# Kernel tuning notes

Measured on AMD Instinct MI355X. Metric: run time of the kernel, lower is better.

## Reference

```python
import jax, jax.numpy as jnp
import numpy as np

N_NODES = 100000
HIDDEN = 128
N_EDGES = 2000000
OUT_DIM = 1


def setup_inputs() -> dict:
    key = jax.random.key(0)
    k1, k2, k3, k4 = jax.random.split(key, 4)
    x_src = jax.random.normal(k1, (N_NODES, HIDDEN), dtype=jnp.float32)
    x_dst = jax.random.normal(k2, (N_NODES, HIDDEN), dtype=jnp.float32)
    edge_label_index = jax.random.randint(k3, (2, N_EDGES), 0, N_NODES, dtype=jnp.int64)
    # nn.Linear(2*hidden, out) params (Kaiming-uniform-ish init scale)
    bound = 1.0 / np.sqrt(2 * HIDDEN)
    weight = jax.random.uniform(k4, (OUT_DIM, 2 * HIDDEN), minval=-bound, maxval=bound, dtype=jnp.float32)
    bias = jnp.zeros((OUT_DIM,), dtype=jnp.float32)
    return {"x_src": x_src, "x_dst": x_dst, "edge_label_index": edge_label_index,
            "weight": weight, "bias": bias}


def reference(x_src, x_dst, edge_label_index, weight, bias):
    # Gather endpoint embeddings: [E, H] each
    h_src = x_src[edge_label_index[0]]
    h_dst = x_dst[edge_label_index[1]]
    # Split the linear over the two halves to avoid materializing the [E, 2H] concat
    w_src, w_dst = weight[:, :HIDDEN], weight[:, HIDDEN:]  # [O, H] each
    out = h_src @ w_src.T + h_dst @ w_dst.T + bias  # [E, O]
    return out
```

## Files before the change

### kernel.cpp

```cpp
#include <hip/hip_runtime.h>

#define HIDDEN  128
#define N_NODES 100000
#define N_EDGES 2000000

typedef float f32x4 __attribute__((ext_vector_type(4)));
typedef int   i32x4 __attribute__((ext_vector_type(4)));

__global__ __launch_bounds__(256) void node_dots_kernel(
    const float* __restrict__ x_src,
    const float* __restrict__ x_dst,
    const float* __restrict__ w,
    float* __restrict__ s_tab,
    float* __restrict__ d_tab)
{
    int gid  = blockIdx.x * 256 + threadIdx.x;
    int node = gid >> 4;
    int lane = gid & 15;
    if (node >= N_NODES) return;

    const f32x4* wv = reinterpret_cast<const f32x4*>(w);
    const f32x4 ws0 = wv[lane];
    const f32x4 ws1 = wv[lane + 16];
    const f32x4 wd0 = wv[lane + 32];
    const f32x4 wd1 = wv[lane + 48];

    const f32x4* xs = reinterpret_cast<const f32x4*>(x_src + (size_t)node * HIDDEN);
    const f32x4* xd = reinterpret_cast<const f32x4*>(x_dst + (size_t)node * HIDDEN);
    const f32x4 a0 = __builtin_nontemporal_load(xs + lane);
    const f32x4 a1 = __builtin_nontemporal_load(xs + lane + 16);
    const f32x4 b0 = __builtin_nontemporal_load(xd + lane);
    const f32x4 b1 = __builtin_nontemporal_load(xd + lane + 16);

    float ss = a0.x*ws0.x + a0.y*ws0.y + a0.z*ws0.z + a0.w*ws0.w
             + a1.x*ws1.x + a1.y*ws1.y + a1.z*ws1.z + a1.w*ws1.w;
    float dd = b0.x*wd0.x + b0.y*wd0.y + b0.z*wd0.z + b0.w*wd0.w
             + b1.x*wd1.x + b1.y*wd1.y + b1.z*wd1.z + b1.w*wd1.w;

    #pragma unroll
    for (int off = 8; off; off >>= 1) {
        ss += __shfl_xor(ss, off);
        dd += __shfl_xor(dd, off);
    }
    if (lane == 0) {
        s_tab[node] = ss;
        d_tab[node] = dd;
    }
}

__global__ __launch_bounds__(256) void edge_kernel(
    const int* __restrict__ idx,
    const float* __restrict__ s_tab,
    const float* __restrict__ d_tab,
    const float* __restrict__ bias,
    float* __restrict__ out)
{
    int t = blockIdx.x * 256 + threadIdx.x;
    if (t >= N_EDGES / 8) return;

    const i32x4* ia = reinterpret_cast<const i32x4*>(idx);
    const i32x4* ib = reinterpret_cast<const i32x4*>(idx + N_EDGES);
    const i32x4 a0 = __builtin_nontemporal_load(ia + 2 * t);
    const i32x4 a1 = __builtin_nontemporal_load(ia + 2 * t + 1);
    const i32x4 b0 = __builtin_nontemporal_load(ib + 2 * t);
    const i32x4 b1 = __builtin_nontemporal_load(ib + 2 * t + 1);
    const float bv = bias[0];

    f32x4 o0, o1;
    o0.x = s_tab[a0.x] + d_tab[b0.x] + bv;
    o0.y = s_tab[a0.y] + d_tab[b0.y] + bv;
    o0.z = s_tab[a0.z] + d_tab[b0.z] + bv;
    o0.w = s_tab[a0.w] + d_tab[b0.w] + bv;
    o1.x = s_tab[a1.x] + d_tab[b1.x] + bv;
    o1.y = s_tab[a1.y] + d_tab[b1.y] + bv;
    o1.z = s_tab[a1.z] + d_tab[b1.z] + bv;
    o1.w = s_tab[a1.w] + d_tab[b1.w] + bv;

    f32x4* ov = reinterpret_cast<f32x4*>(out);
    __builtin_nontemporal_store(o0, ov + 2 * t);
    __builtin_nontemporal_store(o1, ov + 2 * t + 1);
}

extern "C" void kernel_launch(void* const* d_in, const int* in_sizes, int n_in,
                              void* d_out, int out_size, void* d_ws, size_t ws_size,
                              hipStream_t stream) {
    const float* x_src = (const float*)d_in[0];
    const float* x_dst = (const float*)d_in[1];
    const int*   idx   = (const int*)d_in[2];
    const float* w     = (const float*)d_in[3];
    const float* bias  = (const float*)d_in[4];
    float* out = (float*)d_out;

    float* s_tab = (float*)d_ws;
    float* d_tab = s_tab + N_NODES;

    {
        int total_threads = N_NODES * 16;
        int blocks = (total_threads + 255) / 256;
        node_dots_kernel<<<blocks, 256, 0, stream>>>(x_src, x_dst, w, s_tab, d_tab);
    }
    {
        int threads = N_EDGES / 8;
        int blocks = (threads + 255) / 256;
        edge_kernel<<<blocks, 256, 0, stream>>>(idx, s_tab, d_tab, bias, out);
    }
}
```

Baseline: 39.63 us.

## Fuse node-dot and edge kernels into one persistent kernel with grid barrier

Merges the two launches into a single persistent kernel of 512 blocks that uses grid-stride loops. A global atomic-counter barrier separates the node-dot phase from the edge gather phase. The aim is to remove the second kernel launch and the tail gap between kernels. In exchange it needs a memset of the counter, relies on all 512 blocks being co-resident, and cuts parallelism, so fewer loads are in flight for latency hiding.

```diff
diff --git a/kernel.cpp b/kernel.cpp
--- a/kernel.cpp
+++ b/kernel.cpp
@@ -3,21 +3,26 @@
 #define HIDDEN  128
 #define N_NODES 100000
 #define N_EDGES 2000000
+#define NBLK    512
+#define NTHR    256
 
 typedef float f32x4 __attribute__((ext_vector_type(4)));
 typedef int   i32x4 __attribute__((ext_vector_type(4)));
 
-__global__ __launch_bounds__(256) void node_dots_kernel(
+__global__ __launch_bounds__(NTHR) void fused_edge_decoder(
     const float* __restrict__ x_src,
     const float* __restrict__ x_dst,
+    const int*   __restrict__ idx,
     const float* __restrict__ w,
+    const float* __restrict__ bias,
+    float* __restrict__ out,
     float* __restrict__ s_tab,
-    float* __restrict__ d_tab)
+    float* __restrict__ d_tab,
+    int*   __restrict__ barrier_ct)
 {
-    int gid  = blockIdx.x * 256 + threadIdx.x;
-    int node = gid >> 4;
-    int lane = gid & 15;
-    if (node >= N_NODES) return;
+    const int tid      = blockIdx.x * NTHR + threadIdx.x;
+    const int nthreads = NBLK * NTHR;
+    const int lane     = tid & 15;
 
     const f32x4* wv = reinterpret_cast<const f32x4*>(w);
     const f32x4 ws0 = wv[lane];
@@ -25,60 +30,68 @@
     const f32x4 wd0 = wv[lane + 32];
     const f32x4 wd1 = wv[lane + 48];
 
-    const f32x4* xs = reinterpret_cast<const f32x4*>(x_src + (size_t)node * HIDDEN);
-    const f32x4* xd = reinterpret_cast<const f32x4*>(x_dst + (size_t)node * HIDDEN);
-    const f32x4 a0 = __builtin_nontemporal_load(xs + lane);
-    const f32x4 a1 = __builtin_nontemporal_load(xs + lane + 16);
-    const f32x4 b0 = __builtin_nontemporal_load(xd + lane);
-    const f32x4 b1 = __builtin_nontemporal_load(xd + lane + 16);
+    const int group   = tid >> 4;
+    const int ngroups = nthreads >> 4;
 
-    float ss = a0.x*ws0.x + a0.y*ws0.y + a0.z*ws0.z + a0.w*ws0.w
-             + a1.x*ws1.x + a1.y*ws1.y + a1.z*ws1.z + a1.w*ws1.w;
-    float dd = b0.x*wd0.x + b0.y*wd0.y + b0.z*wd0.z + b0.w*wd0.w
-             + b1.x*wd1.x + b1.y*wd1.y + b1.z*wd1.z + b1.w*wd1.w;
+    #pragma unroll 2
+    for (int node = group; node < N_NODES; node += ngroups) {
+        const f32x4* xs = reinterpret_cast<const f32x4*>(x_src + (size_t)node * HIDDEN);
+        const f32x4* xd = reinterpret_cast<const f32x4*>(x_dst + (size_t)node * HIDDEN);
+        const f32x4 a0 = __builtin_nontemporal_load(xs + lane);
+        const f32x4 a1 = __builtin_nontemporal_load(xs + lane + 16);
+        const f32x4 b0 = __builtin_nontemporal_load(xd + lane);
+        const f32x4 b1 = __builtin_nontemporal_load(xd + lane + 16);
 
-    #pragma unroll
-    for (int off = 8; off; off >>= 1) {
-        ss += __shfl_xor(ss, off);
-        dd += __shfl_xor(dd, off);
+        float ss = a0.x*ws0.x + a0.y*ws0.y + a0.z*ws0.z + a0.w*ws0.w
+                 + a1.x*ws1.x + a1.y*ws1.y + a1.z*ws1.z + a1.w*ws1.w;
+        float dd = b0.x*wd0.x + b0.y*wd0.y + b0.z*wd0.z + b0.w*wd0.w
+                 + b1.x*wd1.x + b1.y*wd1.y + b1.z*wd1.z + b1.w*wd1.w;
+
+        #pragma unroll
+        for (int off = 8; off; off >>= 1) {
+            ss += __shfl_xor(ss, off);
+            dd += __shfl_xor(dd, off);
+        }
+        if (lane == 0) {
+            s_tab[node] = ss;
+            d_tab[node] = dd;
+        }
     }
-    if (lane == 0) {
-        s_tab[node] = ss;
-        d_tab[node] = dd;
+
+    __syncthreads();
+    if (threadIdx.x == 0) {
+        __hip_atomic_fetch_add(barrier_ct, 1, __ATOMIC_RELEASE, __HIP_MEMORY_SCOPE_AGENT);
+        while (__hip_atomic_load(barrier_ct, __ATOMIC_ACQUIRE, __HIP_MEMORY_SCOPE_AGENT) < NBLK) {
+            __builtin_amdgcn_s_sleep(1);
+        }
     }
-}
+    __syncthreads();
 
-__global__ __launch_bounds__(256) void edge_kernel(
-    const int* __restrict__ idx,
-    const float* __restrict__ s_tab,
-    const float* __restrict__ d_tab,
-    const float* __restrict__ bias,
-    float* __restrict__ out)
-{
-    int t = blockIdx.x * 256 + threadIdx.x;
-    if (t >= N_EDGES / 8) return;
-
+    const float bv = bias[0];
     const i32x4* ia = reinterpret_cast<const i32x4*>(idx);
     const i32x4* ib = reinterpret_cast<const i32x4*>(idx + N_EDGES);
-    const i32x4 a0 = __builtin_nontemporal_load(ia + 2 * t);
-    const i32x4 a1 = __builtin_nontemporal_load(ia + 2 * t + 1);
-    const i32x4 b0 = __builtin_nontemporal_load(ib + 2 * t);
-    const i32x4 b1 = __builtin_nontemporal_load(ib + 2 * t + 1);
-    const float bv = bias[0];
+    f32x4* ov = reinterpret_cast<f32x4*>(out);
+    const int nt = N_EDGES / 8;
 
-    f32x4 o0, o1;
-    o0.x = s_tab[a0.x] + d_tab[b0.x] + bv;
-    o0.y = s_tab[a0.y] + d_tab[b0.y] + bv;
-    o0.z = s_tab[a0.z] + d_tab[b0.z] + bv;
-    o0.w = s_tab[a0.w] + d_tab[b0.w] + bv;
-    o1.x = s_tab[a1.x] + d_tab[b1.x] + bv;
-    o1.y = s_tab[a1.y] + d_tab[b1.y] + bv;
-    o1.z = s_tab[a1.z] + d_tab[b1.z] + bv;
-    o1.w = s_tab[a1.w] + d_tab[b1.w] + bv;
+    for (int t = tid; t < nt; t += nthreads) {
+        const i32x4 a0 = __builtin_nontemporal_load(ia + 2 * t);
+        const i32x4 a1 = __builtin_nontemporal_load(ia + 2 * t + 1);
+        const i32x4 b0 = __builtin_nontemporal_load(ib + 2 * t);
+        const i32x4 b1 = __builtin_nontemporal_load(ib + 2 * t + 1);
 
-    f32x4* ov = reinterpret_cast<f32x4*>(out);
-    __builtin_nontemporal_store(o0, ov + 2 * t);
-    __builtin_nontemporal_store(o1, ov + 2 * t + 1);
+        f32x4 o0, o1;
+        o0.x = s_tab[a0.x] + d_tab[b0.x] + bv;
+        o0.y = s_tab[a0.y] + d_tab[b0.y] + bv;
+        o0.z = s_tab[a0.z] + d_tab[b0.z] + bv;
+        o0.w = s_tab[a0.w] + d_tab[b0.w] + bv;
+        o1.x = s_tab[a1.x] + d_tab[b1.x] + bv;
+        o1.y = s_tab[a1.y] + d_tab[b1.y] + bv;
+        o1.z = s_tab[a1.z] + d_tab[b1.z] + bv;
+        o1.w = s_tab[a1.w] + d_tab[b1.w] + bv;
+
+        __builtin_nontemporal_store(o0, ov + 2 * t);
+        __builtin_nontemporal_store(o1, ov + 2 * t + 1);
+    }
 }
 
 extern "C" void kernel_launch(void* const* d_in, const int* in_sizes, int n_in,
@@ -93,15 +106,10 @@
 
     float* s_tab = (float*)d_ws;
     float* d_tab = s_tab + N_NODES;
+    int*   barrier_ct = (int*)(d_tab + N_NODES);
 
-    {
-        int total_threads = N_NODES * 16;
-        int blocks = (total_threads + 255) / 256;
-        node_dots_kernel<<<blocks, 256, 0, stream>>>(x_src, x_dst, w, s_tab, d_tab);
-    }
-    {
-        int threads = N_EDGES / 8;
-        int blocks = (threads + 255) / 256;
-        edge_kernel<<<blocks, 256, 0, stream>>>(idx, s_tab, d_tab, bias, out);
-    }
+    hipMemsetAsync(barrier_ct, 0, sizeof(int), stream);
+
+    fused_edge_decoder<<<NBLK, NTHR, 0, stream>>>(
+        x_src, x_dst, idx, w, bias, out, s_tab, d_tab, barrier_ct);
 }
```

Result: slower. 87.09 us (+119.8%).
